# Optimization experiments

Hardware: AMD Instinct MI355X
Metric: run time of the kernel (lower is better)

The kernel has to match this reference:

```python
import jax, jax.numpy as jnp
import numpy as np
import math

N_HEADS = 64
N_KV_HEADS = 8
HEAD_DIM = 128
DIM = 8192
SEQLEN = 2048
KVLEN = 2048
BSZ = 1


def setup_inputs() -> dict:
    key = jax.random.key(0)
    k1, k2, k3, k4, k5 = jax.random.split(key, 5)
    xq = jax.random.normal(k1, (SEQLEN, N_HEADS, BSZ, HEAD_DIM), dtype=jnp.float32)
    keys = jax.random.normal(k2, (BSZ, N_KV_HEADS, KVLEN, HEAD_DIM), dtype=jnp.float32)
    values = jax.random.normal(k3, (BSZ, N_KV_HEADS, KVLEN, HEAD_DIM), dtype=jnp.float32)
    attn_mask = jax.random.normal(k4, (SEQLEN, 1, 1, KVLEN), dtype=jnp.float32)
    wo_w = jax.random.normal(k5, (DIM, DIM), dtype=jnp.float32) * (1.0 / math.sqrt(DIM))
    return {"xq": xq, "keys": keys, "values": values, "attn_mask": attn_mask, "wo_w": wo_w}


def reference(xq, keys, values, attn_mask, wo_w):
    n_rep = N_HEADS // N_KV_HEADS
    bsz = xq.shape[2]
    seqlen = xq.shape[0]
    # repeat_kv: expand kv heads to n_heads (torch expand+reshape == jnp.repeat on head axis)
    k = jnp.repeat(keys, n_rep, axis=1)    # (b, n_heads, kv, d)
    v = jnp.repeat(values, n_rep, axis=1)  # (b, n_heads, kv, d)
    q = jnp.transpose(xq, (2, 1, 0, 3))    # (b, n_heads, s, d)
    mask = jnp.transpose(attn_mask, (2, 1, 0, 3))  # (b_or_1, h_or_1, s, kv)
    scores = jnp.einsum('bhsd,bhtd->bhst', q, k) / math.sqrt(HEAD_DIM)
    scores = scores + mask
    probs = jax.nn.softmax(scores.astype(jnp.float32), axis=-1).astype(q.dtype)
    out = jnp.einsum('bhst,bhtd->bhsd', probs, v)  # (b, h, s, d)
    out = jnp.transpose(out, (0, 2, 1, 3)).reshape(bsz, seqlen, -1)  # (b, s, h*d)
    return out @ wo_w.T  # Linear wo, no bias
```

## Files before the change

kernel.cpp:

```cpp
#include <hip/hip_runtime.h>
#include <hip/hip_bf16.h>
#include <stdint.h>


typedef __bf16 bf16;
typedef __attribute__((ext_vector_type(8))) __bf16 bf16x8;
typedef __attribute__((ext_vector_type(4))) __bf16 bf16x4;
typedef __attribute__((ext_vector_type(4))) float f32x4;
typedef __attribute__((ext_vector_type(16))) float f32x16;
typedef __attribute__((ext_vector_type(4))) unsigned int u32x4;

#define N_HEADS 64
#define N_KVH   8
#define HDIM    128
#define SEQ     2048
#define KVL     2048
#define DIM     8192

__device__ __forceinline__ void gload16(const void* g, void* l) {
  __builtin_amdgcn_global_load_lds((const __attribute__((address_space(1))) void*)g,
                                   (__attribute__((address_space(3))) void*)l,
                                   16, 0, 0);
}

__device__ __forceinline__ unsigned pack2(float lo, float hi) {
  union { bf16 h; unsigned short u; } a, b;
  a.h = (bf16)lo; b.h = (bf16)hi;
  return ((unsigned)b.u << 16) | (unsigned)a.u;
}

__device__ __forceinline__ void exch(unsigned a, unsigned b, unsigned& r0, unsigned& r1) {
  asm("v_permlane32_swap_b32 %0, %1" : "+v"(a), "+v"(b));
  r0 = a; r1 = b;
}

__device__ __forceinline__ void buildfrags(const float (&p)[16], bf16x8& f0, bf16x8& f1) {
  unsigned pk0 = pack2(p[0],  p[1]),  pk1 = pack2(p[2],  p[3]);
  unsigned pk2 = pack2(p[4],  p[5]),  pk3 = pack2(p[6],  p[7]);
  unsigned pk4 = pack2(p[8],  p[9]),  pk5 = pack2(p[10], p[11]);
  unsigned pk6 = pack2(p[12], p[13]), pk7 = pack2(p[14], p[15]);
  unsigned a0, a1, b0, b1, c0, c1, d0, d1;
  exch(pk0, pk2, a0, a1);
  exch(pk1, pk3, b0, b1);
  exch(pk4, pk6, c0, c1);
  exch(pk5, pk7, d0, d1);
  u32x4 w0 = { a0, b0, a1, b1 };
  u32x4 w1 = { c0, d0, c1, d1 };
  f0 = __builtin_bit_cast(bf16x8, w0);
  f1 = __builtin_bit_cast(bf16x8, w1);
}

__global__ void cvt_f32_bf16(const float* __restrict__ in, bf16* __restrict__ out,
                             int n4, float scale) {
  int i = blockIdx.x * blockDim.x + threadIdx.x;
  int stride = gridDim.x * blockDim.x;
  for (; i < n4; i += stride) {
    float4 v = ((const float4*)in)[i];
    bf16x4 o = { (bf16)(v.x * scale), (bf16)(v.y * scale),
                 (bf16)(v.z * scale), (bf16)(v.w * scale) };
    *(bf16x4*)(out + (long)i * 4) = o;
  }
}

__global__ void cvt_vT_kernel(const float* __restrict__ v, bf16* __restrict__ vT) {
  __shared__ bf16 tile[64][132];
  const int tid = threadIdx.x;
  const int kh = blockIdx.x >> 5;
  const int t0 = (blockIdx.x & 31) << 6;
  const float* src = v + ((long)kh * KVL + t0) * HDIM;
#pragma unroll
  for (int it = 0; it < 8; ++it) {
    int q = it * 256 + tid;
    int r = q >> 5;
    int c4 = (q & 31) << 2;
    float4 val = *(const float4*)(src + (long)r * HDIM + c4);
    bf16x4 o = { (bf16)val.x, (bf16)val.y, (bf16)val.z, (bf16)val.w };
    *(bf16x4*)&tile[r][c4] = o;
  }
  __syncthreads();
  const int t = tid & 63;
  const int dbase = tid >> 6;
#pragma unroll
  for (int it = 0; it < 32; ++it) {
    int d = it * 4 + dbase;
    vT[((long)kh * HDIM + d) * KVL + t0 + t] = tile[t][d];
  }
}

__global__ __launch_bounds__(256, 2) void attn_kernel(
    const bf16* __restrict__ qB, const bf16* __restrict__ kB,
    const bf16* __restrict__ vT, const float* __restrict__ mask,
    bf16* __restrict__ attnB)
{
  __shared__ __align__(16) char lds[65536];

  const int tid  = threadIdx.x;
  const int lane = tid & 63;
  const int w    = tid >> 6;
  const int ihi  = lane >> 5;
  const int l31  = lane & 31;

  const int bid = blockIdx.x;
  const int h   = bid >> 4;
  const int q0b = (bid & 15) << 7;
  const int kh  = h >> 3;

#pragma unroll
  for (int rnd = 0; rnd < 8; ++rnd) {
    int row = rnd * 16 + w * 4 + (lane >> 4);
    int cg  = (lane & 15) ^ (row & 15);
    const bf16* g = qB + (((long)(q0b + row) * N_HEADS + h) << 7) + (cg << 3);
    gload16(g, lds + rnd * 4096 + w * 1024);
  }
  __syncthreads();

  bf16x8 qf[8];
  {
    int qrow = (w << 5) + l31;
    const char* qr = lds + qrow * 256;
#pragma unroll
    for (int s = 0; s < 8; ++s)
      qf[s] = *(const bf16x8*)(qr + ((((s << 1) | ihi) ^ (qrow & 15)) << 4));
  }
  __syncthreads();

  {
#pragma unroll
    for (int rnd = 0; rnd < 4; ++rnd) {
      int row = rnd * 16 + w * 4 + (lane >> 4);
      int cg  = (lane & 15) ^ (row & 15);
      const bf16* g = kB + (((long)(kh * KVL + row)) << 7) + (cg << 3);
      gload16(g, lds + rnd * 4096 + w * 1024);
    }
#pragma unroll
    for (int rnd = 0; rnd < 4; ++rnd) {
      int vr = rnd * 16 + w * 4 + (lane >> 4);
      int gg = (lane & 15) ^ (vr & 15);
      int dsrc = (vr << 1) | (gg >> 3);
      const bf16* gp = vT + ((long)(kh * HDIM + dsrc) * KVL) + ((gg & 7) << 3);
      gload16(gp, lds + 32768 + rnd * 4096 + w * 1024);
    }
  }
  __syncthreads();

  const float* mrow = mask + (size_t)(q0b + (w << 5) + l31) * KVL + (ihi << 2);

  f32x16 acc[4];
#pragma unroll
  for (int dt = 0; dt < 4; ++dt) acc[dt] = {};
  float m_run = -1e30f, l_run = 0.f;

  for (int kt = 0; kt < KVL / 64; ++kt) {
    const int cur = kt & 1;
    const int kv0 = kt << 6;

    if (kt < KVL / 64 - 1) {
      const int kv0n = kv0 + 64;
#pragma unroll
      for (int rnd = 0; rnd < 4; ++rnd) {
        int row = rnd * 16 + w * 4 + (lane >> 4);
        int cg  = (lane & 15) ^ (row & 15);
        const bf16* g = kB + (((long)(kh * KVL + kv0n + row)) << 7) + (cg << 3);
        gload16(g, lds + (cur ^ 1) * 16384 + rnd * 4096 + w * 1024);
      }
#pragma unroll
      for (int rnd = 0; rnd < 4; ++rnd) {
        int vr = rnd * 16 + w * 4 + (lane >> 4);
        int gg = (lane & 15) ^ (vr & 15);
        int dsrc = (vr << 1) | (gg >> 3);
        const bf16* gp = vT + ((long)(kh * HDIM + dsrc) * KVL) + kv0n + ((gg & 7) << 3);
        gload16(gp, lds + 32768 + (cur ^ 1) * 16384 + rnd * 4096 + w * 1024);
      }
    }

    const float* mrt = mrow + kv0;
    f32x4 mk0[4], mk1[4];
#pragma unroll
    for (int rq = 0; rq < 4; ++rq) {
      mk0[rq] = *(const f32x4*)(mrt + (rq << 3));
      mk1[rq] = *(const f32x4*)(mrt + 32 + (rq << 3));
    }

    const char* kb = lds + cur * 16384;
    f32x16 s0 = {}, s1 = {};
    const int kr0 = l31, kr1 = 32 + l31;
    __builtin_amdgcn_s_setprio(1);
#pragma unroll
    for (int s = 0; s < 8; ++s) {
      bf16x8 kf0 = *(const bf16x8*)(kb + kr0 * 256 + ((((s << 1) | ihi) ^ (kr0 & 15)) << 4));
      s0 = __builtin_amdgcn_mfma_f32_32x32x16_bf16(kf0, qf[s], s0, 0, 0, 0);
      bf16x8 kf1 = *(const bf16x8*)(kb + kr1 * 256 + ((((s << 1) | ihi) ^ (kr1 & 15)) << 4));
      s1 = __builtin_amdgcn_mfma_f32_32x32x16_bf16(kf1, qf[s], s1, 0, 0, 0);
    }
    __builtin_amdgcn_s_setprio(0);

    float p0[16], p1[16];
#pragma unroll
    for (int rq = 0; rq < 4; ++rq) {
#pragma unroll
      for (int j = 0; j < 4; ++j) {
        p0[rq * 4 + j] = s0[rq * 4 + j] + mk0[rq][j];
        p1[rq * 4 + j] = s1[rq * 4 + j] + mk1[rq][j];
      }
    }

    float q00 = fmaxf(fmaxf(p0[0],  p0[1]),  fmaxf(p0[2],  p0[3]));
    float q01 = fmaxf(fmaxf(p0[4],  p0[5]),  fmaxf(p0[6],  p0[7]));
    float q02 = fmaxf(fmaxf(p0[8],  p0[9]),  fmaxf(p0[10], p0[11]));
    float q03 = fmaxf(fmaxf(p0[12], p0[13]), fmaxf(p0[14], p0[15]));
    float q10 = fmaxf(fmaxf(p1[0],  p1[1]),  fmaxf(p1[2],  p1[3]));
    float q11 = fmaxf(fmaxf(p1[4],  p1[5]),  fmaxf(p1[6],  p1[7]));
    float q12 = fmaxf(fmaxf(p1[8],  p1[9]),  fmaxf(p1[10], p1[11]));
    float q13 = fmaxf(fmaxf(p1[12], p1[13]), fmaxf(p1[14], p1[15]));
    float mx = fmaxf(fmaxf(fmaxf(q00, q01), fmaxf(q02, q03)),
                     fmaxf(fmaxf(q10, q11), fmaxf(q12, q13)));
    mx = fmaxf(mx, __shfl_xor(mx, 32));
    if (!__all((int)(mx - m_run <= 8.0f))) {
      float nm = fmaxf(m_run, mx);
      float al = __expf(m_run - nm);
      m_run = nm;
      l_run *= al;
#pragma unroll
      for (int dt = 0; dt < 4; ++dt) acc[dt] *= al;
    }
    float ps = 0.f;
#pragma unroll
    for (int i = 0; i < 16; ++i) { p0[i] = __expf(p0[i] - m_run); ps += p0[i]; }
#pragma unroll
    for (int i = 0; i < 16; ++i) { p1[i] = __expf(p1[i] - m_run); ps += p1[i]; }
    ps += __shfl_xor(ps, 32);
    l_run += ps;

    bf16x8 pfrag[4];
    buildfrags(p0, pfrag[0], pfrag[1]);
    buildfrags(p1, pfrag[2], pfrag[3]);

    const char* vb = lds + 32768 + cur * 16384;
    const int par8 = (l31 & 1) << 3;
    __builtin_amdgcn_s_setprio(1);
#pragma unroll
    for (int dt = 0; dt < 4; ++dt) {
      const int vrow = (dt << 4) + (l31 >> 1);
      const char* vrp = vb + vrow * 256;
#pragma unroll
      for (int ks = 0; ks < 4; ++ks) {
        int c16 = par8 | (ks << 1) | ihi;
        bf16x8 vf = *(const bf16x8*)(vrp + ((c16 ^ (vrow & 15)) << 4));
        acc[dt] = __builtin_amdgcn_mfma_f32_32x32x16_bf16(vf, pfrag[ks], acc[dt], 0, 0, 0);
      }
    }
    __builtin_amdgcn_s_setprio(0);
    __syncthreads();
  }

  const float linv = 1.0f / l_run;
  char* ep = lds + (w << 13);
#pragma unroll
  for (int dt = 0; dt < 4; ++dt) {
#pragma unroll
    for (int r = 0; r < 16; ++r) {
      int d = (dt << 5) + (r & 3) + ((r >> 2) << 3) + (ihi << 2);
      int byte = l31 * 256 + (((d >> 3) ^ (l31 & 15)) << 4) + ((d & 7) << 1);
      *(bf16*)(ep + byte) = (bf16)(acc[dt][r] * linv);
    }
  }
  __syncthreads();
  const size_t obase = (size_t)(q0b + (w << 5)) * DIM + h * HDIM;
#pragma unroll
  for (int i = 0; i < 8; ++i) {
    int row = (i << 2) + (lane >> 4);
    int cp  = lane & 15;
    int c   = cp ^ (row & 15);
    bf16x8 ov = *(const bf16x8*)(ep + row * 256 + (cp << 4));
    *(bf16x8*)(attnB + obase + (size_t)row * DIM + (c << 3)) = ov;
  }
}

__global__ __launch_bounds__(512, 2) void gemm_bt(
    const bf16* __restrict__ A, const bf16* __restrict__ B, float* __restrict__ C)
{
  __shared__ __align__(16) char lds[131072];
  const int tid  = threadIdx.x;
  const int lane = tid & 63;
  const int w    = tid >> 6;
  const int wm   = w >> 2;
  const int wn   = w & 3;

  const int bid = blockIdx.x;
  const int m0  = (bid >> 5) << 8;
  const int n0  = (((bid & 7) << 2) | ((bid >> 3) & 3)) << 8;

  const int srow = tid >> 3;
  const int sch  = (tid & 7) ^ (srow & 7);
  const bf16* gA0 = A + (long)(m0 + srow) * DIM + (sch << 3);
  const bf16* gB0 = B + (long)(n0 + srow) * DIM + (sch << 3);
  const long rstep = (long)64 * DIM;

  f32x4 acc[8][4];
#pragma unroll
  for (int i = 0; i < 8; ++i)
#pragma unroll
    for (int j = 0; j < 4; ++j) acc[i][j] = { 0.f, 0.f, 0.f, 0.f };

  auto STAGE = [&](int kt) {
    const long ko = (long)kt << 6;
    char* s = lds + (kt & 1) * 65536 + tid * 16;
#pragma unroll
    for (int l = 0; l < 4; ++l)
      gload16(gA0 + l * rstep + ko, s + l * 8192);
#pragma unroll
    for (int l = 0; l < 4; ++l)
      gload16(gB0 + l * rstep + ko, s + 32768 + l * 8192);
  };

  const int g = lane >> 4;
  const int l15 = lane & 15;
  auto COMPUTE = [&](int buf) {
    const char* ab = lds + buf * 65536;
    const char* bb = ab + 32768;
    bf16x8 bfr[4][2];
#pragma unroll
    for (int j = 0; j < 4; ++j) {
      int n = (wn << 6) + (j << 4) + l15;
      const char* nr = bb + n * 128;
#pragma unroll
      for (int ks = 0; ks < 2; ++ks)
        bfr[j][ks] = *(const bf16x8*)(nr + ((((ks << 2) | g) ^ (n & 7)) << 4));
    }
#pragma unroll
    for (int p = 0; p < 4; ++p) {
      bf16x8 af[2][2];
#pragma unroll
      for (int e = 0; e < 2; ++e) {
        int m = (wm << 7) + (((p << 1) | e) << 4) + l15;
        const char* mr = ab + m * 128;
#pragma unroll
        for (int ks = 0; ks < 2; ++ks)
          af[e][ks] = *(const bf16x8*)(mr + ((((ks << 2) | g) ^ (m & 7)) << 4));
      }
      __builtin_amdgcn_s_setprio(1);
#pragma unroll
      for (int e = 0; e < 2; ++e)
#pragma unroll
        for (int j = 0; j < 4; ++j)
#pragma unroll
          for (int ks = 0; ks < 2; ++ks)
            acc[(p << 1) | e][j] =
              __builtin_amdgcn_mfma_f32_16x16x32_bf16(af[e][ks], bfr[j][ks],
                                                      acc[(p << 1) | e][j], 0, 0, 0);
      __builtin_amdgcn_s_setprio(0);
    }
  };

  STAGE(0);
  STAGE(1);

  for (int t = 0; t < 126; ++t) {
    asm volatile("s_waitcnt vmcnt(8)" ::: "memory");
    __builtin_amdgcn_s_barrier();
    COMPUTE(t & 1);
    __builtin_amdgcn_s_barrier();
    STAGE(t + 2);
  }
  asm volatile("s_waitcnt vmcnt(8)" ::: "memory");
  __builtin_amdgcn_s_barrier();
  COMPUTE(0);
  asm volatile("s_waitcnt vmcnt(0)" ::: "memory");
  __builtin_amdgcn_s_barrier();
  COMPUTE(1);

#pragma unroll
  for (int i = 0; i < 8; ++i) {
#pragma unroll
    for (int rr = 0; rr < 4; ++rr) {
      float* cp = C + (long)(m0 + (wm << 7) + (i << 4) + ((lane >> 4) << 2) + rr) * DIM
                    + n0 + (wn << 6) + l15;
#pragma unroll
      for (int j = 0; j < 4; ++j)
        cp[j * 16] = acc[i][j][rr];
    }
  }
}

extern "C" void kernel_launch(void* const* d_in, const int* in_sizes, int n_in,
                              void* d_out, int out_size, void* d_ws, size_t ws_size,
                              hipStream_t stream) {
  const float* xq     = (const float*)d_in[0];
  const float* keys   = (const float*)d_in[1];
  const float* values = (const float*)d_in[2];
  const float* mask   = (const float*)d_in[3];
  const float* wo     = (const float*)d_in[4];
  float* out = (float*)d_out;
  char* ws = (char*)d_ws;

  bf16* woB = (bf16*)ws;
  bf16* qB  = (bf16*)(ws + 134217728ull);
  bf16* kB  = (bf16*)(ws + 134217728ull + 33554432ull);
  bf16* vT  = (bf16*)(ws + 134217728ull + 37748736ull);
  bf16* aB  = (bf16*)(ws + 134217728ull + 41943040ull);

  cvt_f32_bf16<<<dim3(2048), dim3(256), 0, stream>>>(wo, woB, 16777216, 1.0f);
  cvt_f32_bf16<<<dim3(1024), dim3(256), 0, stream>>>(xq, qB, 4194304, 0.08838834764831845f);
  cvt_f32_bf16<<<dim3(256),  dim3(256), 0, stream>>>(keys, kB, 524288, 1.0f);
  cvt_vT_kernel<<<dim3(256), dim3(256), 0, stream>>>(values, vT);
  attn_kernel<<<dim3(1024),  dim3(256), 0, stream>>>(qB, kB, vT, mask, aB);
  gemm_bt<<<dim3(256),       dim3(512), 0, stream>>>(aB, woB, out);
}
```

Measured before the change: 524.5 us.

## Shrink output GEMM tile to 256x128 with BK=32 and launch 512 blocks

Reworks the output projection GEMM from 256x256 tiles with K-step 64 to 256x128 tiles with K-step 32. LDS per block drops from 128KB to 48KB and the grid doubles to 512 blocks, so more blocks can be resident per CU and the grid fills the 256 CUs better. In exchange, each block does half the MFMAs per loaded byte, so global/L2 traffic for A rises. There are also twice as many barrier iterations, each with less compute to hide load latency.

```diff
diff --git a/kernel.cpp b/kernel.cpp
--- a/kernel.cpp
+++ b/kernel.cpp
@@ -279,7 +279,7 @@
 __global__ __launch_bounds__(512, 2) void gemm_bt(
     const bf16* __restrict__ A, const bf16* __restrict__ B, float* __restrict__ C)
 {
-  __shared__ __align__(16) char lds[131072];
+  __shared__ __align__(16) char lds[49152];
   const int tid  = threadIdx.x;
   const int lane = tid & 63;
   const int w    = tid >> 6;
@@ -287,84 +287,72 @@
   const int wn   = w & 3;
 
   const int bid = blockIdx.x;
-  const int m0  = (bid >> 5) << 8;
-  const int n0  = (((bid & 7) << 2) | ((bid >> 3) & 3)) << 8;
-
-  const int srow = tid >> 3;
-  const int sch  = (tid & 7) ^ (srow & 7);
-  const bf16* gA0 = A + (long)(m0 + srow) * DIM + (sch << 3);
-  const bf16* gB0 = B + (long)(n0 + srow) * DIM + (sch << 3);
-  const long rstep = (long)64 * DIM;
-
-  f32x4 acc[8][4];
-#pragma unroll
-  for (int i = 0; i < 8; ++i)
-#pragma unroll
-    for (int j = 0; j < 4; ++j) acc[i][j] = { 0.f, 0.f, 0.f, 0.f };
+  const int m0  = (bid >> 6) << 8;
+  const int n0  = (((bid & 7) << 3) | ((bid >> 3) & 7)) << 7;
+
+  const int sc   = (tid & 7) ^ ((tid >> 3) & 7);
+  const int arow = (tid >> 3) + ((sc >> 2) << 7);
+  const int brow = (tid >> 3) + ((sc >> 2) << 6);
+  const int kc   = (sc & 3) << 3;
+  const bf16* gA = A + (long)(m0 + arow) * DIM + kc;
+  const bf16* gB = B + (long)(n0 + brow) * DIM + kc;
+  const long a1step = (long)64 * DIM;
+
+  f32x4 acc[8][2];
+#pragma unroll
+  for (int i = 0; i < 8; ++i) {
+    acc[i][0] = { 0.f, 0.f, 0.f, 0.f };
+    acc[i][1] = { 0.f, 0.f, 0.f, 0.f };
+  }
 
   auto STAGE = [&](int kt) {
-    const long ko = (long)kt << 6;
-    char* s = lds + (kt & 1) * 65536 + tid * 16;
-#pragma unroll
-    for (int l = 0; l < 4; ++l)
-      gload16(gA0 + l * rstep + ko, s + l * 8192);
-#pragma unroll
-    for (int l = 0; l < 4; ++l)
-      gload16(gB0 + l * rstep + ko, s + 32768 + l * 8192);
+    const long ko = (long)kt << 5;
+    char* s = lds + (kt & 1) * 24576 + tid * 16;
+    gload16(gA + ko, s);
+    gload16(gA + a1step + ko, s + 8192);
+    gload16(gB + ko, s + 16384);
   };
 
   const int g = lane >> 4;
   const int l15 = lane & 15;
   auto COMPUTE = [&](int buf) {
-    const char* ab = lds + buf * 65536;
-    const char* bb = ab + 32768;
-    bf16x8 bfr[4][2];
-#pragma unroll
-    for (int j = 0; j < 4; ++j) {
-      int n = (wn << 6) + (j << 4) + l15;
-      const char* nr = bb + n * 128;
-#pragma unroll
-      for (int ks = 0; ks < 2; ++ks)
-        bfr[j][ks] = *(const bf16x8*)(nr + ((((ks << 2) | g) ^ (n & 7)) << 4));
-    }
-#pragma unroll
-    for (int p = 0; p < 4; ++p) {
-      bf16x8 af[2][2];
-#pragma unroll
-      for (int e = 0; e < 2; ++e) {
-        int m = (wm << 7) + (((p << 1) | e) << 4) + l15;
-        const char* mr = ab + m * 128;
-#pragma unroll
-        for (int ks = 0; ks < 2; ++ks)
-          af[e][ks] = *(const bf16x8*)(mr + ((((ks << 2) | g) ^ (m & 7)) << 4));
-      }
-      __builtin_amdgcn_s_setprio(1);
-#pragma unroll
-      for (int e = 0; e < 2; ++e)
-#pragma unroll
-        for (int j = 0; j < 4; ++j)
-#pragma unroll
-          for (int ks = 0; ks < 2; ++ks)
-            acc[(p << 1) | e][j] =
-              __builtin_amdgcn_mfma_f32_16x16x32_bf16(af[e][ks], bfr[j][ks],
-                                                      acc[(p << 1) | e][j], 0, 0, 0);
-      __builtin_amdgcn_s_setprio(0);
-    }
+    const char* ab = lds + buf * 24576;
+    const char* bb = ab + 16384;
+    bf16x8 bfr[2];
+#pragma unroll
+    for (int j = 0; j < 2; ++j) {
+      int n = (wn << 5) + (j << 4) + l15;
+      int p = n & 63;
+      int c = ((n >> 6) << 2) | g;
+      bfr[j] = *(const bf16x8*)(bb + p * 128 + ((c ^ (p & 7)) << 4));
+    }
+    __builtin_amdgcn_s_setprio(1);
+#pragma unroll
+    for (int i = 0; i < 8; ++i) {
+      int m = (wm << 7) + (i << 4) + l15;
+      int p = m & 127;
+      int c = ((m >> 7) << 2) | g;
+      bf16x8 af = *(const bf16x8*)(ab + p * 128 + ((c ^ (p & 7)) << 4));
+      acc[i][0] = __builtin_amdgcn_mfma_f32_16x16x32_bf16(af, bfr[0], acc[i][0], 0, 0, 0);
+      acc[i][1] = __builtin_amdgcn_mfma_f32_16x16x32_bf16(af, bfr[1], acc[i][1], 0, 0, 0);
+    }
+    __builtin_amdgcn_s_setprio(0);
   };
 
   STAGE(0);
   STAGE(1);
 
-  for (int t = 0; t < 126; ++t) {
-    asm volatile("s_waitcnt vmcnt(8)" ::: "memory");
+  for (int t = 0; t < 254; ++t) {
+    asm volatile("s_waitcnt vmcnt(3)" ::: "memory");
     __builtin_amdgcn_s_barrier();
     COMPUTE(t & 1);
     __builtin_amdgcn_s_barrier();
     STAGE(t + 2);
   }
-  asm volatile("s_waitcnt vmcnt(8)" ::: "memory");
+  asm volatile("s_waitcnt vmcnt(3)" ::: "memory");
   __builtin_amdgcn_s_barrier();
   COMPUTE(0);
+  __builtin_amdgcn_s_barrier();
   asm volatile("s_waitcnt vmcnt(0)" ::: "memory");
   __builtin_amdgcn_s_barrier();
   COMPUTE(1);
@@ -374,10 +362,9 @@
 #pragma unroll
     for (int rr = 0; rr < 4; ++rr) {
       float* cp = C + (long)(m0 + (wm << 7) + (i << 4) + ((lane >> 4) << 2) + rr) * DIM
-                    + n0 + (wn << 6) + l15;
-#pragma unroll
-      for (int j = 0; j < 4; ++j)
-        cp[j * 16] = acc[i][j][rr];
+                    + n0 + (wn << 5) + l15;
+      cp[0]  = acc[i][0][rr];
+      cp[16] = acc[i][1][rr];
     }
   }
 }
@@ -404,5 +391,5 @@
   cvt_f32_bf16<<<dim3(256),  dim3(256), 0, stream>>>(keys, kB, 524288, 1.0f);
   cvt_vT_kernel<<<dim3(256), dim3(256), 0, stream>>>(values, vT);
   attn_kernel<<<dim3(1024),  dim3(256), 0, stream>>>(qB, kB, vT, mask, aB);
-  gemm_bt<<<dim3(256),       dim3(512), 0, stream>>>(aB, woB, out);
-}
+  gemm_bt<<<dim3(512),       dim3(512), 0, stream>>>(aB, woB, out);
+}
```

After: 556.3 us. +6.1%, slower.
